# Optimization experiments

Measured on AMD Instinct MI355X. Metric: run time of the kernel, lower is better.

Reference implementation:

```python
import jax, jax.numpy as jnp
import numpy as np

V, B, F = 4, 8192, 128  # views, batch, fea_out
EPS = 1e-5  # torch BatchNorm1d default eps


def setup_inputs() -> dict:
    key = jax.random.key(0)
    k1, k2 = jax.random.split(key)
    x = jax.random.normal(k1, (V, B, F), dtype=jnp.float32)
    # Linear(F*F -> F) weight/bias; scale ~ kaiming-ish to keep activations sane
    W = jax.random.normal(k2, (F, F * F), dtype=jnp.float32) * 0.01
    b = jnp.zeros((F,), dtype=jnp.float32)
    gamma = jnp.ones((F,), dtype=jnp.float32)   # BN weight
    beta = jnp.zeros((F,), dtype=jnp.float32)   # BN bias
    return {"x": x, "W": W, "b": b, "gamma": gamma, "beta": beta}


def reference(x, W, b, gamma, beta):
    # x: [V, B, F] stack of views. Original loops over pairs (i<j):
    #   outer = x[i][:, :, None] @ x[j][:, None, :]          -> [B, F, F]
    #   flat  = outer.view(B, F*F)   (flat index = i*F + j)
    #   out   = ReLU(BN(Linear(flat)))
    # We fuse: Linear(flat(outer)) == einsum over W reshaped to [F_out, F, F],
    # avoiding the [B, F*F] intermediate. Same math.
    Vn, Bn, Fn = x.shape
    ii, jj = np.triu_indices(Vn, k=1)          # P = V*(V-1)/2 pairs
    x1 = x[ii]                                  # [P, B, F]
    x2 = x[jj]                                  # [P, B, F]
    Wr = W.reshape(Fn, Fn, Fn)                  # [F_out, F_i, F_j], matches row-major flatten
    # bilinear form per pair/batch: y[p,b,o] = sum_ij x1[p,b,i] * Wr[o,i,j] * x2[p,b,j] + b[o]
    y = jnp.einsum('pbi,oij,pbj->pbo', x1, Wr, x2) + b
    # BatchNorm1d in training mode: per-call batch stats (over batch axis, per pair),
    # biased variance, then affine, then ReLU.
    mean = jnp.mean(y, axis=1, keepdims=True)
    var = jnp.var(y, axis=1, keepdims=True)
    y_hat = (y - mean) * jax.lax.rsqrt(var + EPS)
    out = jax.nn.relu(gamma * y_hat + beta)     # [P, B, F]
    return out
```

## Files before the change

### kernel.cpp

```cpp
#include <hip/hip_runtime.h>

#define Fdim 128
#define Bsz  8192
#define Pn   6
#define EPSI 1e-5f
#define X2P 136
#define X1P 72

typedef _Float16 half8  __attribute__((ext_vector_type(8)));
typedef _Float16 half4t __attribute__((ext_vector_type(4)));
typedef float    float4t __attribute__((ext_vector_type(4)));

__constant__ int PAIR_A[6] = {0,0,0,1,1,2};
__constant__ int PAIR_B[6] = {1,2,3,2,3,3};

__global__ __launch_bounds__(256) void wprep(const float* __restrict__ W,
                                             _Float16* __restrict__ Wws) {
    int t    = blockIdx.x * 256 + threadIdx.x;
    int c    = t >> 9;
    int r    = t & 511;
    int nt   = r >> 6;
    int lane = r & 63;
    int q    = lane >> 4;
    int ol   = lane & 15;
    int o    = nt * 16 + ol;
    const float4t* src = (const float4t*)(W + (size_t)o * 16384 + c * 32 + q * 8);
    float4t a0 = src[0];
    float4t a1 = src[1];
    half8 h;
    h[0] = (_Float16)a0[0]; h[1] = (_Float16)a0[1];
    h[2] = (_Float16)a0[2]; h[3] = (_Float16)a0[3];
    h[4] = (_Float16)a1[0]; h[5] = (_Float16)a1[1];
    h[6] = (_Float16)a1[2]; h[7] = (_Float16)a1[3];
    *(half8*)(Wws + (size_t)t * 8) = h;
}

__global__ __launch_bounds__(256, 3) void gemm(const float* __restrict__ x,
                                               const _Float16* __restrict__ Wws,
                                               _Float16* __restrict__ yws,
                                               float* __restrict__ ssum,
                                               float* __restrict__ ssq) {
    __shared__ _Float16 x2t[128 * X2P];
    __shared__ _Float16 x1th[128 * X1P];

    int bid  = blockIdx.x;
    int p    = bid >> 7;
    int rem  = bid & 127;
    int mblk = rem >> 1;
    int nh   = rem & 1;
    int m0   = mblk * 128;
    int v1   = PAIR_A[p];
    int v2   = PAIR_B[p];
    int tid  = threadIdx.x;

    {
        const float4t* s2p = (const float4t*)(x + ((size_t)v2 * Bsz + m0) * Fdim);
        for (int it = 0; it < 16; ++it) {
            int idx = it * 256 + tid;
            int row = idx >> 5;
            int col = (idx & 31) * 4;
            float4t b = s2p[idx];
            half4t h2; h2[0]=(_Float16)b[0]; h2[1]=(_Float16)b[1];
                       h2[2]=(_Float16)b[2]; h2[3]=(_Float16)b[3];
            *(half4t*)&x2t[row * X2P + col] = h2;
        }
    }

    int lane  = tid & 63;
    int w     = tid >> 6;
    int wrow  = w >> 1;
    int wcol  = w & 1;
    int ol    = lane & 15;
    int q     = lane >> 4;
    int ntg0  = nh * 4 + wcol * 2;
    int ntg1  = ntg0 + 1;
    int rbase = wrow * 64;

    float4t acc[4][2];
#pragma unroll
    for (int mt = 0; mt < 4; ++mt) {
        acc[mt][0] = (float4t){0.f, 0.f, 0.f, 0.f};
        acc[mt][1] = (float4t){0.f, 0.f, 0.f, 0.f};
    }

    const half8* wb = (const half8*)Wws;
    const size_t woff0 = (size_t)ntg0 * 64 + lane;
    const size_t woff1 = (size_t)ntg1 * 64 + lane;
    const float* x1src = x + ((size_t)v1 * Bsz + m0) * Fdim;

    for (int kh = 0; kh < 2; ++kh) {
        if (kh) __syncthreads();
        for (int it = 0; it < 8; ++it) {
            int idx = it * 256 + tid;
            int row = idx >> 4;
            int c4  = (idx & 15) * 4;
            float4t a = *(const float4t*)(x1src + (size_t)row * Fdim + kh * 64 + c4);
            half4t h1; h1[0]=(_Float16)a[0]; h1[1]=(_Float16)a[1];
                       h1[2]=(_Float16)a[2]; h1[3]=(_Float16)a[3];
            *(half4t*)&x1th[row * X1P + c4] = h1;
        }
        __syncthreads();

        int ibase = kh * 64;
        for (int jc = 0; jc < 4; ++jc) {
            half8 x2f[4];
#pragma unroll
            for (int mt = 0; mt < 4; ++mt)
                x2f[mt] = *(const half8*)&x2t[(rbase + mt * 16 + ol) * X2P + jc * 32 + q * 8];

            half8 bfa0 = wb[(size_t)((ibase + 0) * 4 + jc) * 512 + woff0];
            half8 bfa1 = wb[(size_t)((ibase + 0) * 4 + jc) * 512 + woff1];
            half8 bfb0 = wb[(size_t)((ibase + 1) * 4 + jc) * 512 + woff0];
            half8 bfb1 = wb[(size_t)((ibase + 1) * 4 + jc) * 512 + woff1];

            for (int i8 = 0; i8 < 8; ++i8) {
                half8 x1f[4];
#pragma unroll
                for (int mt = 0; mt < 4; ++mt)
                    x1f[mt] = *(const half8*)&x1th[(rbase + mt * 16 + ol) * X1P + i8 * 8];
#pragma unroll
                for (int ii = 0; ii < 8; ++ii) {
                    int il  = i8 * 8 + ii;
                    int ipl = (il < 62) ? (il + 2) : 63;
                    half8 bn0 = wb[(size_t)((ibase + ipl) * 4 + jc) * 512 + woff0];
                    half8 bn1 = wb[(size_t)((ibase + ipl) * 4 + jc) * 512 + woff1];
#pragma unroll
                    for (int mt = 0; mt < 4; ++mt) {
                        _Float16 sc = x1f[mt][ii];
                        half8 a = x2f[mt] * sc;
                        acc[mt][0] = __builtin_amdgcn_mfma_f32_16x16x32_f16(a, bfa0, acc[mt][0], 0, 0, 0);
                        acc[mt][1] = __builtin_amdgcn_mfma_f32_16x16x32_f16(a, bfa1, acc[mt][1], 0, 0, 0);
                    }
                    bfa0 = bfb0; bfa1 = bfb1;
                    bfb0 = bn0;  bfb1 = bn1;
                }
            }
        }
    }

    float sum0 = 0.f, sq0 = 0.f, sum1 = 0.f, sq1 = 0.f;
    int col0 = ntg0 * 16 + ol;
    int col1 = ntg1 * 16 + ol;
#pragma unroll
    for (int mt = 0; mt < 4; ++mt) {
#pragma unroll
        for (int r = 0; r < 4; ++r) {
            size_t row = (size_t)p * Bsz + m0 + rbase + mt * 16 + q * 4 + r;
            float v0 = acc[mt][0][r];
            sum0 += v0; sq0 += v0 * v0;
            yws[row * Fdim + col0] = (_Float16)v0;
            float v1e = acc[mt][1][r];
            sum1 += v1e; sq1 += v1e * v1e;
            yws[row * Fdim + col1] = (_Float16)v1e;
        }
    }
    sum0 += __shfl_xor(sum0, 16, 64);  sum0 += __shfl_xor(sum0, 32, 64);
    sq0  += __shfl_xor(sq0, 16, 64);   sq0  += __shfl_xor(sq0, 32, 64);
    sum1 += __shfl_xor(sum1, 16, 64);  sum1 += __shfl_xor(sum1, 32, 64);
    sq1  += __shfl_xor(sq1, 16, 64);   sq1  += __shfl_xor(sq1, 32, 64);
    if (q == 0) {
        atomicAdd(&ssum[p * Fdim + col0], sum0);
        atomicAdd(&ssq [p * Fdim + col0], sq0);
        atomicAdd(&ssum[p * Fdim + col1], sum1);
        atomicAdd(&ssq [p * Fdim + col1], sq1);
    }
}

__global__ __launch_bounds__(256) void bnrelu(const _Float16* __restrict__ yws,
                                              const float* __restrict__ ssum,
                                              const float* __restrict__ ssq,
                                              const float* __restrict__ gamma,
                                              const float* __restrict__ beta,
                                              float* __restrict__ out) {
    __shared__ float gs[128], sh[128];
    size_t ebase = (size_t)blockIdx.x * 1024;
    int p = (int)(ebase >> 20);
    int t = threadIdx.x;
    if (t < 128) {
        float mean = ssum[p * Fdim + t] * (1.0f / 8192.0f);
        float var  = ssq [p * Fdim + t] * (1.0f / 8192.0f) - mean * mean;
        float g    = gamma[t] * rsqrtf(var + EPSI);
        gs[t] = g;
        sh[t] = beta[t] - g * mean;
    }
    __syncthreads();
    size_t e0 = ebase + (size_t)t * 4;
    int o0 = (int)(e0 & 127);
    half4t y = *(const half4t*)(yws + e0);
    float4t r;
#pragma unroll
    for (int l = 0; l < 4; ++l) {
        float v = fmaf(gs[o0 + l], (float)y[l], sh[o0 + l]);
        r[l] = v > 0.f ? v : 0.f;
    }
    *(float4t*)(out + e0) = r;
}

extern "C" void kernel_launch(void* const* d_in, const int* in_sizes, int n_in,
                              void* d_out, int out_size, void* d_ws, size_t ws_size,
                              hipStream_t stream) {
    const float* x     = (const float*)d_in[0];
    const float* W     = (const float*)d_in[1];
    const float* gamma = (const float*)d_in[3];
    const float* beta  = (const float*)d_in[4];
    float* out = (float*)d_out;

    char* ws = (char*)d_ws;
    _Float16* yws = (_Float16*)ws;
    _Float16* Wws = (_Float16*)(ws + 12582912);
    float*    ssum = (float*)(ws + 16777216);
    float*    ssq  = ssum + Pn * Fdim;

    (void)hipMemsetAsync(ssum, 0, 2 * Pn * Fdim * sizeof(float), stream);
    wprep<<<1024, 256, 0, stream>>>(W, Wws);
    gemm<<<768, 256, 0, stream>>>(x, Wws, yws, ssum, ssq);
    bnrelu<<<6144, 256, 0, stream>>>(yws, ssum, ssq, gamma, beta, out);
}
```

Measured before the change: 258.9 us.

## Switch bilinear GEMM to 32x32x16 MFMA and fold stat zeroing into wprep

Each wave now computes a 32-row by 64-column tile using two 32x32x16 MFMAs per i-step, replacing eight 16x16x32 MFMAs over a 64x32 tile. The W prep layout and the epilogue row mapping change to match the new MFMA fragment layout. This cuts the per-element scaling multiplies and LDS fragment loads per MFMA, but it also changes W reuse per wave. The separate memset of the BN stat buffers is removed, and the zeroing is done by the last wprep block instead.

Result: slower. 324.0 us (+25.2%).

```diff
diff --git a/kernel.cpp b/kernel.cpp
--- a/kernel.cpp
+++ b/kernel.cpp
@@ -9,22 +9,23 @@
 
 typedef _Float16 half8  __attribute__((ext_vector_type(8)));
 typedef _Float16 half4t __attribute__((ext_vector_type(4)));
-typedef float    float4t __attribute__((ext_vector_type(4)));
+typedef float    float4t  __attribute__((ext_vector_type(4)));
+typedef float    float16t __attribute__((ext_vector_type(16)));
 
 __constant__ int PAIR_A[6] = {0,0,0,1,1,2};
 __constant__ int PAIR_B[6] = {1,2,3,2,3,3};
 
 __global__ __launch_bounds__(256) void wprep(const float* __restrict__ W,
-                                             _Float16* __restrict__ Wws) {
+                                             _Float16* __restrict__ Wws,
+                                             float* __restrict__ szero) {
     int t    = blockIdx.x * 256 + threadIdx.x;
-    int c    = t >> 9;
-    int r    = t & 511;
+    int c16  = t >> 8;
+    int r    = t & 255;
     int nt   = r >> 6;
     int lane = r & 63;
-    int q    = lane >> 4;
-    int ol   = lane & 15;
-    int o    = nt * 16 + ol;
-    const float4t* src = (const float4t*)(W + (size_t)o * 16384 + c * 32 + q * 8);
+    int q2   = lane >> 5;
+    int o    = nt * 32 + (lane & 31);
+    const float4t* src = (const float4t*)(W + (size_t)o * 16384 + c16 * 16 + q2 * 8);
     float4t a0 = src[0];
     float4t a1 = src[1];
     half8 h;
@@ -33,6 +34,9 @@
     h[4] = (_Float16)a1[0]; h[5] = (_Float16)a1[1];
     h[6] = (_Float16)a1[2]; h[7] = (_Float16)a1[3];
     *(half8*)(Wws + (size_t)t * 8) = h;
+    if (blockIdx.x == 1023) {
+        for (int z = 0; z < 6; ++z) szero[threadIdx.x + 256 * z] = 0.f;
+    }
 }
 
 __global__ __launch_bounds__(256, 3) void gemm(const float* __restrict__ x,
@@ -68,20 +72,15 @@
 
     int lane  = tid & 63;
     int w     = tid >> 6;
-    int wrow  = w >> 1;
-    int wcol  = w & 1;
-    int ol    = lane & 15;
-    int q     = lane >> 4;
-    int ntg0  = nh * 4 + wcol * 2;
+    int ol32  = lane & 31;
+    int q2    = lane >> 5;
+    int rbase = w * 32;
+    int ntg0  = nh * 2;
     int ntg1  = ntg0 + 1;
-    int rbase = wrow * 64;
-
-    float4t acc[4][2];
-#pragma unroll
-    for (int mt = 0; mt < 4; ++mt) {
-        acc[mt][0] = (float4t){0.f, 0.f, 0.f, 0.f};
-        acc[mt][1] = (float4t){0.f, 0.f, 0.f, 0.f};
-    }
+
+    float16t acc0 = {0.f}, acc1 = {0.f};
+#pragma unroll
+    for (int z = 0; z < 16; ++z) { acc0[z] = 0.f; acc1[z] = 0.f; }
 
     const half8* wb = (const half8*)Wws;
     const size_t woff0 = (size_t)ntg0 * 64 + lane;
@@ -102,35 +101,26 @@
         __syncthreads();
 
         int ibase = kh * 64;
-        for (int jc = 0; jc < 4; ++jc) {
-            half8 x2f[4];
-#pragma unroll
-            for (int mt = 0; mt < 4; ++mt)
-                x2f[mt] = *(const half8*)&x2t[(rbase + mt * 16 + ol) * X2P + jc * 32 + q * 8];
-
-            half8 bfa0 = wb[(size_t)((ibase + 0) * 4 + jc) * 512 + woff0];
-            half8 bfa1 = wb[(size_t)((ibase + 0) * 4 + jc) * 512 + woff1];
-            half8 bfb0 = wb[(size_t)((ibase + 1) * 4 + jc) * 512 + woff0];
-            half8 bfb1 = wb[(size_t)((ibase + 1) * 4 + jc) * 512 + woff1];
+        for (int jc = 0; jc < 8; ++jc) {
+            half8 x2f = *(const half8*)&x2t[(rbase + ol32) * X2P + jc * 16 + q2 * 8];
+
+            half8 bfa0 = wb[(size_t)((ibase + 0) * 8 + jc) * 256 + woff0];
+            half8 bfa1 = wb[(size_t)((ibase + 0) * 8 + jc) * 256 + woff1];
+            half8 bfb0 = wb[(size_t)((ibase + 1) * 8 + jc) * 256 + woff0];
+            half8 bfb1 = wb[(size_t)((ibase + 1) * 8 + jc) * 256 + woff1];
 
             for (int i8 = 0; i8 < 8; ++i8) {
-                half8 x1f[4];
-#pragma unroll
-                for (int mt = 0; mt < 4; ++mt)
-                    x1f[mt] = *(const half8*)&x1th[(rbase + mt * 16 + ol) * X1P + i8 * 8];
+                half8 x1f = *(const half8*)&x1th[(rbase + ol32) * X1P + i8 * 8];
 #pragma unroll
                 for (int ii = 0; ii < 8; ++ii) {
                     int il  = i8 * 8 + ii;
                     int ipl = (il < 62) ? (il + 2) : 63;
-                    half8 bn0 = wb[(size_t)((ibase + ipl) * 4 + jc) * 512 + woff0];
-                    half8 bn1 = wb[(size_t)((ibase + ipl) * 4 + jc) * 512 + woff1];
-#pragma unroll
-                    for (int mt = 0; mt < 4; ++mt) {
-                        _Float16 sc = x1f[mt][ii];
-                        half8 a = x2f[mt] * sc;
-                        acc[mt][0] = __builtin_amdgcn_mfma_f32_16x16x32_f16(a, bfa0, acc[mt][0], 0, 0, 0);
-                        acc[mt][1] = __builtin_amdgcn_mfma_f32_16x16x32_f16(a, bfa1, acc[mt][1], 0, 0, 0);
-                    }
+                    half8 bn0 = wb[(size_t)((ibase + ipl) * 8 + jc) * 256 + woff0];
+                    half8 bn1 = wb[(size_t)((ibase + ipl) * 8 + jc) * 256 + woff1];
+                    _Float16 sc = x1f[ii];
+                    half8 a = x2f * sc;
+                    acc0 = __builtin_amdgcn_mfma_f32_32x32x16_f16(a, bfa0, acc0, 0, 0, 0);
+                    acc1 = __builtin_amdgcn_mfma_f32_32x32x16_f16(a, bfa1, acc1, 0, 0, 0);
                     bfa0 = bfb0; bfa1 = bfb1;
                     bfb0 = bn0;  bfb1 = bn1;
                 }
@@ -139,26 +129,22 @@
     }
 
     float sum0 = 0.f, sq0 = 0.f, sum1 = 0.f, sq1 = 0.f;
-    int col0 = ntg0 * 16 + ol;
-    int col1 = ntg1 * 16 + ol;
-#pragma unroll
-    for (int mt = 0; mt < 4; ++mt) {
-#pragma unroll
-        for (int r = 0; r < 4; ++r) {
-            size_t row = (size_t)p * Bsz + m0 + rbase + mt * 16 + q * 4 + r;
-            float v0 = acc[mt][0][r];
-            sum0 += v0; sq0 += v0 * v0;
-            yws[row * Fdim + col0] = (_Float16)v0;
-            float v1e = acc[mt][1][r];
-            sum1 += v1e; sq1 += v1e * v1e;
-            yws[row * Fdim + col1] = (_Float16)v1e;
-        }
-    }
-    sum0 += __shfl_xor(sum0, 16, 64);  sum0 += __shfl_xor(sum0, 32, 64);
-    sq0  += __shfl_xor(sq0, 16, 64);   sq0  += __shfl_xor(sq0, 32, 64);
-    sum1 += __shfl_xor(sum1, 16, 64);  sum1 += __shfl_xor(sum1, 32, 64);
-    sq1  += __shfl_xor(sq1, 16, 64);   sq1  += __shfl_xor(sq1, 32, 64);
-    if (q == 0) {
+    int col0 = ntg0 * 32 + ol32;
+    int col1 = ntg1 * 32 + ol32;
+#pragma unroll
+    for (int reg = 0; reg < 16; ++reg) {
+        int rl = (reg & 3) + 4 * q2 + 8 * (reg >> 2);
+        size_t row = (size_t)p * Bsz + m0 + rbase + rl;
+        float v0 = acc0[reg];
+        sum0 += v0; sq0 += v0 * v0;
+        yws[row * Fdim + col0] = (_Float16)v0;
+        float v1e = acc1[reg];
+        sum1 += v1e; sq1 += v1e * v1e;
+        yws[row * Fdim + col1] = (_Float16)v1e;
+    }
+    sum0 += __shfl_xor(sum0, 32, 64);  sq0 += __shfl_xor(sq0, 32, 64);
+    sum1 += __shfl_xor(sum1, 32, 64);  sq1 += __shfl_xor(sq1, 32, 64);
+    if (q2 == 0) {
         atomicAdd(&ssum[p * Fdim + col0], sum0);
         atomicAdd(&ssq [p * Fdim + col0], sq0);
         atomicAdd(&ssum[p * Fdim + col1], sum1);
@@ -211,8 +197,7 @@
     float*    ssum = (float*)(ws + 16777216);
     float*    ssq  = ssum + Pn * Fdim;
 
-    (void)hipMemsetAsync(ssum, 0, 2 * Pn * Fdim * sizeof(float), stream);
-    wprep<<<1024, 256, 0, stream>>>(W, Wws);
+    wprep<<<1024, 256, 0, stream>>>(W, Wws, ssum);
     gemm<<<768, 256, 0, stream>>>(x, Wws, yws, ssum, ssq);
     bnrelu<<<6144, 256, 0, stream>>>(yws, ssum, ssq, gamma, beta, out);
 }
```
